# Kernel optimization log

Measured on AMD Instinct MI355X. Metric: run time of the kernel, lower is better.

The kernel has to match this reference:

```python
import jax, jax.numpy as jnp
import numpy as np
import math

B, T, C = 2, 2048, 1024
H = 16
D = C // H

def setup_inputs() -> dict:
    key = jax.random.key(0)
    k1, k2, k3, k4, k5 = jax.random.split(key, 5)
    scale = 0.02
    return {
        "x": jax.random.normal(k1, (B, T, C), dtype=jnp.float32),
        "w_attn": jax.random.normal(k2, (3 * C, C), dtype=jnp.float32) * scale,
        "b_attn": jax.random.normal(k3, (3 * C,), dtype=jnp.float32) * scale,
        "w_proj": jax.random.normal(k4, (C, C), dtype=jnp.float32) * scale,
        "b_proj": jax.random.normal(k5, (C,), dtype=jnp.float32) * scale,
    }

def reference(x, w_attn, b_attn, w_proj, b_proj):
    b, t, c = x.shape
    # c_attn: torch Linear -> x @ W.T + b, output [b, t, 3c]
    qkv = jnp.einsum('btc,fc->btf', x, w_attn) + b_attn
    # einops 'b t (a h d) -> a b h t d' with a=3, h=H
    qkv = qkv.reshape(b, t, 3, H, D).transpose(2, 0, 3, 1, 4)
    q, k, v = qkv[0], qkv[1], qkv[2]  # each [b, h, t, d]
    att = jnp.einsum('bhtd,bhsd->bhts', q, k) * (1.0 / math.sqrt(D))
    # causal mask: positions s > t are masked
    mask = jnp.tril(jnp.ones((t, t), dtype=bool))
    att = jnp.where(mask[None, None, :, :], att, jnp.float32(-jnp.inf))
    att = jax.nn.softmax(att, axis=-1)
    y = jnp.einsum('bhts,bhsd->bhtd', att, v)  # [b, h, t, d]
    y = y.transpose(0, 2, 1, 3).reshape(b, t, c)
    return jnp.einsum('btc,fc->btf', y, w_proj) + b_proj
```

## Files before the change

kernel.cpp:

```cpp
#include <hip/hip_runtime.h>
#include <stdint.h>

typedef unsigned short u16;
typedef __attribute__((ext_vector_type(8))) __bf16 bvec8;
typedef __attribute__((ext_vector_type(4))) float f32x4;

__device__ __forceinline__ u16 f32_to_bf16(float f) {
    uint32_t u = __float_as_uint(f);
    u += 0x7fffu + ((u >> 16) & 1u);
    return (u16)(u >> 16);
}

__device__ __forceinline__ void gl2lds16(const u16* g, u16* l) {
    void* gnc = const_cast<void*>((const void*)g);
    __builtin_amdgcn_global_load_lds(
        (__attribute__((address_space(1))) uint32_t*)gnc,
        (__attribute__((address_space(3))) uint32_t*)((void*)l),
        16, 0, 0);
}

__global__ __launch_bounds__(256) void cvt3(
    const float* __restrict__ a, int na4, const float* __restrict__ b, int nb4,
    const float* __restrict__ c, int nc4,
    u16* __restrict__ oa, u16* __restrict__ ob, u16* __restrict__ oc)
{
    int i = blockIdx.x * 256 + threadIdx.x;
    const float* src; u16* dst; int off;
    if (i < na4)             { src = a; dst = oa; off = i; }
    else if (i < na4 + nb4)  { src = b; dst = ob; off = i - na4; }
    else if (i < na4 + nb4 + nc4) { src = c; dst = oc; off = i - na4 - nb4; }
    else return;
    float4 v = ((const float4*)src)[off];
    ushort4 o;
    o.x = f32_to_bf16(v.x); o.y = f32_to_bf16(v.y);
    o.z = f32_to_bf16(v.z); o.w = f32_to_bf16(v.w);
    ((ushort4*)dst)[off] = o;
}

template <int BNt, bool OUT_BF16>
__global__ __launch_bounds__(256) void gemm_bt_bias(
    const u16* __restrict__ A, const u16* __restrict__ B,
    const float* __restrict__ bias, void* __restrict__ Cv,
    int M, int N, int K)
{
    constexpr int NT = BNt / 32;
    __shared__ __attribute__((aligned(16))) u16 As[128 * 32];
    __shared__ __attribute__((aligned(16))) u16 Bs[BNt * 32];

    const int tid = threadIdx.x, wave = tid >> 6, lane = tid & 63;
    const int col = lane & 15, quad = lane >> 4;
    const int m0 = blockIdx.y * 128, n0 = blockIdx.x * BNt;
    const int wm = (wave >> 1) * 64, wn = (wave & 1) * (BNt / 2);
    const int srow = lane >> 2, schunk = lane & 3;
    const u16* Ag = A + (size_t)(m0 + wave * 32) * K;

    f32x4 acc[4][NT];
#pragma unroll
    for (int i = 0; i < 4; i++)
#pragma unroll
        for (int j = 0; j < NT; j++) acc[i][j] = f32x4{0.f, 0.f, 0.f, 0.f};

    for (int k0 = 0; k0 < K; k0 += 32) {
        __syncthreads();
        gl2lds16(Ag + (size_t)(srow)      * K + k0 + schunk * 8, &As[(wave * 2 + 0) * 512]);
        gl2lds16(Ag + (size_t)(16 + srow) * K + k0 + schunk * 8, &As[(wave * 2 + 1) * 512]);
        if constexpr (BNt == 128) {
            const u16* Bg = B + (size_t)(n0 + wave * 32) * K;
            gl2lds16(Bg + (size_t)(srow)      * K + k0 + schunk * 8, &Bs[(wave * 2 + 0) * 512]);
            gl2lds16(Bg + (size_t)(16 + srow) * K + k0 + schunk * 8, &Bs[(wave * 2 + 1) * 512]);
        } else {
            const u16* Bg = B + (size_t)(n0 + wave * 16) * K;
            gl2lds16(Bg + (size_t)(srow)      * K + k0 + schunk * 8, &Bs[wave * 512]);
        }
        __syncthreads();

        bvec8 af[4], bfv[NT];
#pragma unroll
        for (int mt = 0; mt < 4; mt++)  af[mt]  = *(const bvec8*)&As[(wm + mt * 16 + col) * 32 + quad * 8];
#pragma unroll
        for (int nt = 0; nt < NT; nt++) bfv[nt] = *(const bvec8*)&Bs[(wn + nt * 16 + col) * 32 + quad * 8];
#pragma unroll
        for (int mt = 0; mt < 4; mt++)
#pragma unroll
            for (int nt = 0; nt < NT; nt++)
                acc[mt][nt] = __builtin_amdgcn_mfma_f32_16x16x32_bf16(af[mt], bfv[nt], acc[mt][nt], 0, 0, 0);
    }

#pragma unroll
    for (int mt = 0; mt < 4; mt++) {
#pragma unroll
        for (int r = 0; r < 4; r++) {
            const int m = m0 + wm + mt * 16 + quad * 4 + r;
#pragma unroll
            for (int nt = 0; nt < NT; nt++) {
                const int n = n0 + wn + nt * 16 + col;
                float v = acc[mt][nt][r] + bias[n];
                if (OUT_BF16) ((u16*)Cv)[(size_t)m * N + n] = f32_to_bf16(v);
                else          ((float*)Cv)[(size_t)m * N + n] = v;
            }
        }
    }
}

__global__ __launch_bounds__(256) void transpose_v(const u16* __restrict__ qkv,
                                                   u16* __restrict__ vT)
{
    __shared__ u16 Ts[64 * 74];
    const int tid = threadIdx.x;
    const int t0 = blockIdx.x * 64, h = blockIdx.y, b = blockIdx.z;
    const u16* src = qkv + (size_t)b * 2048 * 3072 + 2048 + h * 64;
#pragma unroll
    for (int k2 = 0; k2 < 2; k2++) {
        int c = k2 * 256 + tid, tl = c >> 3, ch = c & 7;
        *(uint4*)&Ts[tl * 74 + ch * 8] = *(const uint4*)(src + (size_t)(t0 + tl) * 3072 + ch * 8);
    }
    __syncthreads();
    u16* dst = vT + (size_t)((b * 16 + h) * 64) * 2048;
#pragma unroll
    for (int k2 = 0; k2 < 2; k2++) {
        int c = k2 * 256 + tid, d = c >> 3, tch = c & 7;
        u16 tmp[8];
#pragma unroll
        for (int j2 = 0; j2 < 8; j2++) tmp[j2] = Ts[(tch * 8 + j2) * 74 + d];
        *(uint4*)&dst[(size_t)d * 2048 + t0 + tch * 8] = *(const uint4*)tmp;
    }
}

__global__ __launch_bounds__(256) void attn_kernel(const u16* __restrict__ qkv,
                                                   const u16* __restrict__ vT,
                                                   u16* __restrict__ Y)
{
    __shared__ __attribute__((aligned(16))) u16 Qs[64 * 64];
    __shared__ __attribute__((aligned(16))) u16 Ks[2][64 * 64];
    __shared__ __attribute__((aligned(16))) u16 Vs[2][64 * 64];
    __shared__ __attribute__((aligned(16))) u16 Ps[4 * 16 * 72];

    const int tid = threadIdx.x, wave = tid >> 6, lane = tid & 63;
    const int col = lane & 15, quad = lane >> 4;

    const int g = blockIdx.x;
    const int b = g >> 4, h = g & 15;
    const int s_idx = blockIdx.y;

    const u16* qb = qkv + (size_t)b * 2048 * 3072;
    const u16* vb = vT + (size_t)g * 64 * 2048;

    const int c0 = wave * 64 + lane, c1 = 256 + c0;
    const int r0 = c0 >> 3, p0 = c0 & 7, r1 = c1 >> 3, p1 = c1 & 7;
    const int sw0 = (p0 ^ (r0 & 7)) * 8, sw1 = (p1 ^ (r1 & 7)) * 8;

    const int tloc = wave * 16 + quad * 4;

#pragma unroll
    for (int phase = 0; phase < 2; ++phase) {
        const int qt = phase ? (31 - s_idx) : s_idx;
        const int q0 = qt * 64;

        __syncthreads();
        gl2lds16(qb + (size_t)(q0 + r0) * 3072 + h * 64 + sw0, &Qs[wave * 512]);
        gl2lds16(qb + (size_t)(q0 + r1) * 3072 + h * 64 + sw1, &Qs[2048 + wave * 512]);
        __syncthreads();

        const int qrow = wave * 16 + col;
        bvec8 qf0 = *(const bvec8*)&Qs[qrow * 64 + ((quad       ^ (qrow & 7)) * 8)];
        bvec8 qf1 = *(const bvec8*)&Qs[qrow * 64 + (((4 + quad) ^ (qrow & 7)) * 8)];

        float l_acc[4] = {0.f, 0.f, 0.f, 0.f};
        f32x4 o[4];
#pragma unroll
        for (int d = 0; d < 4; d++) o[d] = f32x4{0.f, 0.f, 0.f, 0.f};

        {
            gl2lds16(qb + (size_t)(r0) * 3072 + 1024 + h * 64 + sw0, &Ks[0][wave * 512]);
            gl2lds16(qb + (size_t)(r1) * 3072 + 1024 + h * 64 + sw1, &Ks[0][2048 + wave * 512]);
            gl2lds16(vb + (size_t)r0 * 2048 + sw0, &Vs[0][wave * 512]);
            gl2lds16(vb + (size_t)r1 * 2048 + sw1, &Vs[0][2048 + wave * 512]);
        }

        for (int kt = 0; kt <= qt; ++kt) {
            const int cur = kt & 1;
            if (kt < qt) {
                const int s0n = (kt + 1) * 64;
                const int nb2 = cur ^ 1;
                gl2lds16(qb + (size_t)(s0n + r0) * 3072 + 1024 + h * 64 + sw0, &Ks[nb2][wave * 512]);
                gl2lds16(qb + (size_t)(s0n + r1) * 3072 + 1024 + h * 64 + sw1, &Ks[nb2][2048 + wave * 512]);
                gl2lds16(vb + (size_t)r0 * 2048 + s0n + sw0, &Vs[nb2][wave * 512]);
                gl2lds16(vb + (size_t)r1 * 2048 + s0n + sw1, &Vs[nb2][2048 + wave * 512]);
                asm volatile("s_waitcnt vmcnt(4)" ::: "memory");
            } else {
                asm volatile("s_waitcnt vmcnt(0)" ::: "memory");
            }
            asm volatile("s_barrier" ::: "memory");

            f32x4 sv[4];
#pragma unroll
            for (int nt = 0; nt < 4; nt++) {
                const int krow = nt * 16 + col;
                bvec8 kf0 = *(const bvec8*)&Ks[cur][krow * 64 + ((quad       ^ (krow & 7)) * 8)];
                bvec8 kf1 = *(const bvec8*)&Ks[cur][krow * 64 + (((4 + quad) ^ (krow & 7)) * 8)];
                sv[nt] = f32x4{0.f, 0.f, 0.f, 0.f};
                sv[nt] = __builtin_amdgcn_mfma_f32_16x16x32_bf16(qf0, kf0, sv[nt], 0, 0, 0);
                sv[nt] = __builtin_amdgcn_mfma_f32_16x16x32_bf16(qf1, kf1, sv[nt], 0, 0, 0);
            }

            const bool diag = (kt == qt);
            u16* pw = &Ps[wave * 16 * 72];
#pragma unroll
            for (int nt = 0; nt < 4; nt++) {
#pragma unroll
                for (int r = 0; r < 4; r++) {
                    float p = __expf(sv[nt][r] * 0.125f);
                    if (diag && (nt * 16 + col) > (tloc + r)) p = 0.f;
                    l_acc[r] += p;
                    pw[(quad * 4 + r) * 72 + nt * 16 + col] = f32_to_bf16(p);
                }
            }

#pragma unroll
            for (int ks = 0; ks < 2; ks++) {
                bvec8 pf = *(const bvec8*)&Ps[wave * 16 * 72 + col * 72 + ks * 32 + quad * 8];
#pragma unroll
                for (int d = 0; d < 4; d++) {
                    const int vrow = d * 16 + col;
                    bvec8 vf = *(const bvec8*)&Vs[cur][vrow * 64 + (((ks * 4 + quad) ^ (vrow & 7)) * 8)];
                    o[d] = __builtin_amdgcn_mfma_f32_16x16x32_bf16(pf, vf, o[d], 0, 0, 0);
                }
            }
            asm volatile("s_barrier" ::: "memory");
        }

#pragma unroll
        for (int r = 0; r < 4; r++) {
            float s = l_acc[r];
            s += __shfl_xor(s, 1); s += __shfl_xor(s, 2);
            s += __shfl_xor(s, 4); s += __shfl_xor(s, 8);
            const float inv = 1.0f / s;
            const int t = q0 + wave * 16 + quad * 4 + r;
#pragma unroll
            for (int d = 0; d < 4; d++)
                Y[(size_t)(b * 2048 + t) * 1024 + h * 64 + d * 16 + col] =
                    f32_to_bf16(o[d][r] * inv);
        }
    }
}

extern "C" void kernel_launch(void* const* d_in, const int* in_sizes, int n_in,
                              void* d_out, int out_size, void* d_ws, size_t ws_size,
                              hipStream_t stream) {
    const float* x      = (const float*)d_in[0];
    const float* w_attn = (const float*)d_in[1];
    const float* b_attn = (const float*)d_in[2];
    const float* w_proj = (const float*)d_in[3];
    const float* b_proj = (const float*)d_in[4];
    float* out = (float*)d_out;

    u16* xb  = (u16*)d_ws;
    u16* wab = xb  + (size_t)4096 * 1024;
    u16* wpb = wab + (size_t)3072 * 1024;
    u16* qkv = wpb + (size_t)1024 * 1024;
    u16* y   = qkv + (size_t)4096 * 3072;
    u16* vT  = xb;

    const int na4 = 4096 * 1024 / 4, nb4 = 3072 * 1024 / 4, nc4 = 1024 * 1024 / 4;
    cvt3<<<(na4 + nb4 + nc4 + 255) / 256, 256, 0, stream>>>(
        x, na4, w_attn, nb4, w_proj, nc4, xb, wab, wpb);

    dim3 g1(3072 / 128, 4096 / 128);
    gemm_bt_bias<128, true><<<g1, 256, 0, stream>>>(xb, wab, b_attn, qkv, 4096, 3072, 1024);

    dim3 gt(32, 16, 2);
    transpose_v<<<gt, 256, 0, stream>>>(qkv, vT);

    dim3 g2(32, 16, 1);
    attn_kernel<<<g2, 256, 0, stream>>>(qkv, vT, y);

    dim3 g3(1024 / 64, 4096 / 128);
    gemm_bt_bias<64, false><<<g3, 256, 0, stream>>>(y, wpb, b_proj, out, 4096, 1024, 1024);
}
```

Measured before the change: 193.1 us.

## Switch attention to 32x32 MFMA with split-key waves and register-resident P

Reworks the attention kernel so each wave computes a 32x32 query-by-key tile with 32x32x16 MFMAs, with the four waves arranged as 2 query halves by 2 key halves. P stays in registers as packed bf16 operands instead of making a round trip through shared memory, and the two key-half partial outputs and row sums are combined through LDS at the end. It also skips the fully masked diagonal sub-tile and permutes the V-transpose reads. The intent is fewer LDS stores and loads and higher MFMA efficiency per wave, at the cost of an end-of-tile cross-wave reduction and idle waves on the diagonal block.

```diff
diff --git a/kernel.cpp b/kernel.cpp
--- a/kernel.cpp
+++ b/kernel.cpp
@@ -1,14 +1,21 @@
 #include <hip/hip_runtime.h>
+#include <hip/hip_bf16.h>
 #include <stdint.h>
 
 typedef unsigned short u16;
 typedef __attribute__((ext_vector_type(8))) __bf16 bvec8;
 typedef __attribute__((ext_vector_type(4))) float f32x4;
+typedef __attribute__((ext_vector_type(16))) float f32x16;
 
 __device__ __forceinline__ u16 f32_to_bf16(float f) {
     uint32_t u = __float_as_uint(f);
     u += 0x7fffu + ((u >> 16) & 1u);
     return (u16)(u >> 16);
+}
+__device__ __forceinline__ uint32_t pack_bf16x2(float lo, float hi) {
+    union { __hip_bfloat162 h; uint32_t u; } c;
+    c.h = __float22bfloat162_rn(make_float2(lo, hi));
+    return c.u;
 }
 
 __device__ __forceinline__ void gl2lds16(const u16* g, u16* l) {
@@ -121,7 +128,11 @@
         int c = k2 * 256 + tid, d = c >> 3, tch = c & 7;
         u16 tmp[8];
 #pragma unroll
-        for (int j2 = 0; j2 < 8; j2++) tmp[j2] = Ts[(tch * 8 + j2) * 74 + d];
+        for (int j2 = 0; j2 < 8; j2++) {
+            int p  = tch * 8 + j2;
+            int sl = (p & 32) | ((p & 1) << 4) | ((p >> 1) & 15);
+            tmp[j2] = Ts[sl * 74 + d];
+        }
         *(uint4*)&dst[(size_t)d * 2048 + t0 + tch * 8] = *(const uint4*)tmp;
     }
 }
@@ -133,10 +144,12 @@
     __shared__ __attribute__((aligned(16))) u16 Qs[64 * 64];
     __shared__ __attribute__((aligned(16))) u16 Ks[2][64 * 64];
     __shared__ __attribute__((aligned(16))) u16 Vs[2][64 * 64];
-    __shared__ __attribute__((aligned(16))) u16 Ps[4 * 16 * 72];
+    __shared__ __attribute__((aligned(16))) float Obuf[2][64][36];
+    __shared__ __attribute__((aligned(16))) float Lbuf[2][2][32];
 
     const int tid = threadIdx.x, wave = tid >> 6, lane = tid & 63;
-    const int col = lane & 15, quad = lane >> 4;
+    const int l31 = lane & 31, hi = lane >> 5;
+    const int wq = wave >> 1, ws = wave & 1;
 
     const int g = blockIdx.x;
     const int b = g >> 4, h = g & 15;
@@ -146,10 +159,11 @@
     const u16* vb = vT + (size_t)g * 64 * 2048;
 
     const int c0 = wave * 64 + lane, c1 = 256 + c0;
-    const int r0 = c0 >> 3, p0 = c0 & 7, r1 = c1 >> 3, p1 = c1 & 7;
-    const int sw0 = (p0 ^ (r0 & 7)) * 8, sw1 = (p1 ^ (r1 & 7)) * 8;
-
-    const int tloc = wave * 16 + quad * 4;
+    const int r0 = c0 >> 3, p0c = c0 & 7, r1 = c1 >> 3, p1c = c1 & 7;
+    const int sw0 = (p0c ^ (r0 & 7)) * 8, sw1 = (p1c ^ (r1 & 7)) * 8;
+
+    const int q_lane = wq * 32 + l31;
+    const int s_lane = ws * 32 + l31;
 
 #pragma unroll
     for (int phase = 0; phase < 2; ++phase) {
@@ -159,29 +173,27 @@
         __syncthreads();
         gl2lds16(qb + (size_t)(q0 + r0) * 3072 + h * 64 + sw0, &Qs[wave * 512]);
         gl2lds16(qb + (size_t)(q0 + r1) * 3072 + h * 64 + sw1, &Qs[2048 + wave * 512]);
-        __syncthreads();
-
-        const int qrow = wave * 16 + col;
-        bvec8 qf0 = *(const bvec8*)&Qs[qrow * 64 + ((quad       ^ (qrow & 7)) * 8)];
-        bvec8 qf1 = *(const bvec8*)&Qs[qrow * 64 + (((4 + quad) ^ (qrow & 7)) * 8)];
-
-        float l_acc[4] = {0.f, 0.f, 0.f, 0.f};
-        f32x4 o[4];
-#pragma unroll
-        for (int d = 0; d < 4; d++) o[d] = f32x4{0.f, 0.f, 0.f, 0.f};
-
-        {
-            gl2lds16(qb + (size_t)(r0) * 3072 + 1024 + h * 64 + sw0, &Ks[0][wave * 512]);
-            gl2lds16(qb + (size_t)(r1) * 3072 + 1024 + h * 64 + sw1, &Ks[0][2048 + wave * 512]);
-            gl2lds16(vb + (size_t)r0 * 2048 + sw0, &Vs[0][wave * 512]);
-            gl2lds16(vb + (size_t)r1 * 2048 + sw1, &Vs[0][2048 + wave * 512]);
-        }
+        gl2lds16(qb + (size_t)(r0) * 3072 + 1024 + h * 64 + sw0, &Ks[0][wave * 512]);
+        gl2lds16(qb + (size_t)(r1) * 3072 + 1024 + h * 64 + sw1, &Ks[0][2048 + wave * 512]);
+        gl2lds16(vb + (size_t)r0 * 2048 + sw0, &Vs[0][wave * 512]);
+        gl2lds16(vb + (size_t)r1 * 2048 + sw1, &Vs[0][2048 + wave * 512]);
+        asm volatile("s_waitcnt vmcnt(4)" ::: "memory");
+        asm volatile("s_barrier" ::: "memory");
+
+        bvec8 qf[4];
+#pragma unroll
+        for (int c = 0; c < 4; c++)
+            qf[c] = *(const bvec8*)&Qs[q_lane * 64 + (((c * 2 + hi) ^ (q_lane & 7)) * 8)];
+
+        float l_acc = 0.f;
+        f32x16 o0, o1;
+#pragma unroll
+        for (int i = 0; i < 16; i++) { o0[i] = 0.f; o1[i] = 0.f; }
 
         for (int kt = 0; kt <= qt; ++kt) {
             const int cur = kt & 1;
             if (kt < qt) {
-                const int s0n = (kt + 1) * 64;
-                const int nb2 = cur ^ 1;
+                const int s0n = (kt + 1) * 64, nb2 = cur ^ 1;
                 gl2lds16(qb + (size_t)(s0n + r0) * 3072 + 1024 + h * 64 + sw0, &Ks[nb2][wave * 512]);
                 gl2lds16(qb + (size_t)(s0n + r1) * 3072 + 1024 + h * 64 + sw1, &Ks[nb2][2048 + wave * 512]);
                 gl2lds16(vb + (size_t)r0 * 2048 + s0n + sw0, &Vs[nb2][wave * 512]);
@@ -192,54 +204,104 @@
             }
             asm volatile("s_barrier" ::: "memory");
 
-            f32x4 sv[4];
-#pragma unroll
-            for (int nt = 0; nt < 4; nt++) {
-                const int krow = nt * 16 + col;
-                bvec8 kf0 = *(const bvec8*)&Ks[cur][krow * 64 + ((quad       ^ (krow & 7)) * 8)];
-                bvec8 kf1 = *(const bvec8*)&Ks[cur][krow * 64 + (((4 + quad) ^ (krow & 7)) * 8)];
-                sv[nt] = f32x4{0.f, 0.f, 0.f, 0.f};
-                sv[nt] = __builtin_amdgcn_mfma_f32_16x16x32_bf16(qf0, kf0, sv[nt], 0, 0, 0);
-                sv[nt] = __builtin_amdgcn_mfma_f32_16x16x32_bf16(qf1, kf1, sv[nt], 0, 0, 0);
-            }
-
             const bool diag = (kt == qt);
-            u16* pw = &Ps[wave * 16 * 72];
-#pragma unroll
-            for (int nt = 0; nt < 4; nt++) {
-#pragma unroll
-                for (int r = 0; r < 4; r++) {
-                    float p = __expf(sv[nt][r] * 0.125f);
-                    if (diag && (nt * 16 + col) > (tloc + r)) p = 0.f;
-                    l_acc[r] += p;
-                    pw[(quad * 4 + r) * 72 + nt * 16 + col] = f32_to_bf16(p);
-                }
-            }
-
-#pragma unroll
-            for (int ks = 0; ks < 2; ks++) {
-                bvec8 pf = *(const bvec8*)&Ps[wave * 16 * 72 + col * 72 + ks * 32 + quad * 8];
-#pragma unroll
-                for (int d = 0; d < 4; d++) {
-                    const int vrow = d * 16 + col;
-                    bvec8 vf = *(const bvec8*)&Vs[cur][vrow * 64 + (((ks * 4 + quad) ^ (vrow & 7)) * 8)];
-                    o[d] = __builtin_amdgcn_mfma_f32_16x16x32_bf16(pf, vf, o[d], 0, 0, 0);
+            if (!(diag && wq == 0 && ws == 1)) {
+                f32x16 sv;
+#pragma unroll
+                for (int i = 0; i < 16; i++) sv[i] = 0.f;
+#pragma unroll
+                for (int c = 0; c < 4; c++) {
+                    bvec8 kf = *(const bvec8*)&Ks[cur][s_lane * 64 + (((c * 2 + hi) ^ (s_lane & 7)) * 8)];
+                    sv = __builtin_amdgcn_mfma_f32_32x32x16_bf16(kf, qf[c], sv, 0, 0, 0);
+                }
+
+                float pv[16];
+                if (diag) {
+                    const int s_base = kt * 64 + ws * 32 + 4 * hi;
+                    const int q_act  = q0 + wq * 32 + l31;
+#pragma unroll
+                    for (int i = 0; i < 16; i++) {
+                        float p = exp2f(sv[i] * 0.1803368801f);
+                        int s_act = s_base + (i & 3) + 8 * (i >> 2);
+                        if (s_act > q_act) p = 0.f;
+                        pv[i] = p;
+                    }
+                } else {
+#pragma unroll
+                    for (int i = 0; i < 16; i++)
+                        pv[i] = exp2f(sv[i] * 0.1803368801f);
+                }
+                {
+                    float t0a = (pv[0] + pv[1]) + (pv[2] + pv[3]);
+                    float t1a = (pv[4] + pv[5]) + (pv[6] + pv[7]);
+                    float t2a = (pv[8] + pv[9]) + (pv[10] + pv[11]);
+                    float t3a = (pv[12] + pv[13]) + (pv[14] + pv[15]);
+                    l_acc += (t0a + t1a) + (t2a + t3a);
+                }
+
+                uint32_t w[8];
+#pragma unroll
+                for (int i = 0; i < 8; i++) w[i] = pack_bf16x2(pv[i], pv[i + 8]);
+                union { uint32_t u[4]; bvec8 v; } pf0, pf1;
+                pf0.u[0] = w[0]; pf0.u[1] = w[1]; pf0.u[2] = w[2]; pf0.u[3] = w[3];
+                pf1.u[0] = w[4]; pf1.u[1] = w[5]; pf1.u[2] = w[6]; pf1.u[3] = w[7];
+
+#pragma unroll
+                for (int ch = 0; ch < 2; ch++) {
+                    bvec8 pf = ch ? pf1.v : pf0.v;
+                    const int lc = ws * 4 + ch * 2 + hi;
+                    const int d0r = l31;
+                    bvec8 vf0 = *(const bvec8*)&Vs[cur][d0r * 64 + ((lc ^ (d0r & 7)) * 8)];
+                    o0 = __builtin_amdgcn_mfma_f32_32x32x16_bf16(pf, vf0, o0, 0, 0, 0);
+                    const int d1r = 32 + l31;
+                    bvec8 vf1 = *(const bvec8*)&Vs[cur][d1r * 64 + ((lc ^ (d1r & 7)) * 8)];
+                    o1 = __builtin_amdgcn_mfma_f32_32x32x16_bf16(pf, vf1, o1, 0, 0, 0);
                 }
             }
             asm volatile("s_barrier" ::: "memory");
         }
 
-#pragma unroll
-        for (int r = 0; r < 4; r++) {
-            float s = l_acc[r];
-            s += __shfl_xor(s, 1); s += __shfl_xor(s, 2);
-            s += __shfl_xor(s, 4); s += __shfl_xor(s, 8);
-            const float inv = 1.0f / s;
-            const int t = q0 + wave * 16 + quad * 4 + r;
-#pragma unroll
-            for (int d = 0; d < 4; d++)
-                Y[(size_t)(b * 2048 + t) * 1024 + h * 64 + d * 16 + col] =
-                    f32_to_bf16(o[d][r] * inv);
+        l_acc += __shfl_xor(l_acc, 32);
+        __syncthreads();
+        if (lane < 32) Lbuf[ws][wq][lane] = l_acc;
+        if (ws == 0) {
+#pragma unroll
+            for (int nt = 0; nt < 2; nt++) {
+                const int d = nt * 32 + l31;
+#pragma unroll
+                for (int g4 = 0; g4 < 4; g4++) {
+                    f32x4 v;
+#pragma unroll
+                    for (int j = 0; j < 4; j++) v[j] = nt ? o1[g4 * 4 + j] : o0[g4 * 4 + j];
+                    *(f32x4*)&Obuf[wq][d][8 * g4 + 4 * hi] = v;
+                }
+            }
+        }
+        __syncthreads();
+        if (ws == 1) {
+            float inv[16];
+#pragma unroll
+            for (int g4 = 0; g4 < 4; g4++) {
+                f32x4 la = *(const f32x4*)&Lbuf[0][wq][8 * g4 + 4 * hi];
+                f32x4 lb = *(const f32x4*)&Lbuf[1][wq][8 * g4 + 4 * hi];
+#pragma unroll
+                for (int j = 0; j < 4; j++) inv[g4 * 4 + j] = 1.0f / (la[j] + lb[j]);
+            }
+#pragma unroll
+            for (int nt = 0; nt < 2; nt++) {
+                const int d = nt * 32 + l31;
+#pragma unroll
+                for (int g4 = 0; g4 < 4; g4++) {
+                    f32x4 po = *(const f32x4*)&Obuf[wq][d][8 * g4 + 4 * hi];
+#pragma unroll
+                    for (int j = 0; j < 4; j++) {
+                        const int i = g4 * 4 + j;
+                        float val = ((nt ? o1[i] : o0[i]) + po[j]) * inv[i];
+                        const int t = q0 + wq * 32 + 8 * g4 + 4 * hi + j;
+                        Y[(size_t)(b * 2048 + t) * 1024 + h * 64 + d] = f32_to_bf16(val);
+                    }
+                }
+            }
         }
     }
 }
```

New measurement: 194.3 us. Within noise of the previous version (+0.6%).
